# Kernel tuning notes

Hardware: AMD Instinct MI355X
Metric: run time of the kernel (lower is better)

The kernel has to match this reference:

```python
import jax, jax.numpy as jnp
import numpy as np

L, N, H, SQ = 24, 16384, 128, 32
D_OP, D_ATTR, D_FILT, D_OUT = 16, 56, 74, 32
D_IN = 2 * SQ + D_OP + D_ATTR  # 136
EPS = 1e-5
SLOPE = 0.01  # LeakyReLU default


def setup_inputs() -> dict:
    key = jax.random.key(0)
    ks = jax.random.split(key, 24)
    f32 = jnp.float32
    inp = {
        'op_pad': jax.random.normal(ks[0], (L, N, D_OP), f32),
        'attr_pad': jax.random.normal(ks[1], (L, N, D_ATTR), f32),
        'filter_pad': jax.random.normal(ks[2], (L, N, D_FILT), f32),
        'output_pad': jax.random.normal(ks[3], (L, N, D_OUT), f32),
        'mapping_pad': jax.random.randint(ks[4], (L, N, 2), 0, N + 1, jnp.int32),
        'batch_size': 4096,
        # filter / output squeeze linears
        'Wf': jax.random.normal(ks[5], (SQ, D_FILT), f32) * 0.05,
        'bf': jax.random.normal(ks[6], (SQ,), f32) * 0.05,
        'Wo': jax.random.normal(ks[7], (SQ, D_OUT), f32) * 0.05,
        'bo': jax.random.normal(ks[8], (SQ,), f32) * 0.05,
        # batchnorm affine params
        'g1': jnp.ones((SQ,), f32), 'beta1': jnp.zeros((SQ,), f32),
        'g2': jnp.ones((SQ,), f32), 'beta2': jnp.zeros((SQ,), f32),
        # LSTM (PyTorch layout: gates i,f,g,o stacked)
        'Wih': jax.random.normal(ks[9], (4 * H, D_IN), f32) * 0.05,
        'Whh': jax.random.normal(ks[10], (4 * H, H), f32) * 0.05,
        'bih': jax.random.normal(ks[11], (4 * H,), f32) * 0.05,
        'bhh': jax.random.normal(ks[12], (4 * H,), f32) * 0.05,
        # final MLP head
        'W1': jax.random.normal(ks[13], (20, H), f32) * 0.05,
        'b1': jax.random.normal(ks[14], (20,), f32) * 0.05,
        'W2': jax.random.normal(ks[15], (1, 20), f32) * 0.05,
        'b2': jax.random.normal(ks[16], (1,), f32) * 0.05,
    }
    return inp


def _leaky(x):
    return jnp.where(x > 0, x, SLOPE * x)


def _bn(x, g, b):
    # BatchNorm1d in training mode: batch stats (biased var), eps=1e-5
    m = jnp.mean(x, axis=0)
    v = jnp.var(x, axis=0)
    return (x - m) * jax.lax.rsqrt(v + EPS) * g + b


def _forward(op_pad, attr_pad, filter_pad, output_pad, mapping_pad, batch_size,
             Wf, bf, Wo, bo, g1, beta1, g2, beta2, Wih, Whh, bih, bhh, W1, b1, W2, b2):
    l, n = op_pad.shape[0], op_pad.shape[1]
    # squeeze filter / output features, flattened over (L*N)
    fd = _bn(_leaky(filter_pad.reshape(l * n, -1) @ Wf.T + bf), g1, beta1).reshape(l, n, SQ)
    od = _bn(_leaky(output_pad.reshape(l * n, -1) @ Wo.T + bo), g2, beta2).reshape(l, n, SQ)
    lstm_in = jnp.concatenate([op_pad, attr_pad, fd, od], axis=2)  # [L,N,D_IN]

    def step(carry, xs):
        h, c = carry                       # [N,H] previous level states
        x, mapping = xs                    # [N,D_IN], [N,2]
        mask = (mapping != 0)[..., None]   # [N,2,1]
        idx = jnp.maximum(mapping - 1, 0)  # [N,2] gather indices
        gh = jnp.sum(jnp.where(mask, h[idx], 0.0), axis=1) * 0.5  # [N,H]
        gc = jnp.sum(jnp.where(mask, c[idx], 0.0), axis=1) * 0.5
        gates = x @ Wih.T + bih + gh @ Whh.T + bhh  # [N,4H]
        i, f, g, o = jnp.split(gates, 4, axis=1)
        c_new = jax.nn.sigmoid(f) * gc + jax.nn.sigmoid(i) * jnp.tanh(g)
        h_new = jax.nn.sigmoid(o) * jnp.tanh(c_new)
        return (h_new, c_new), None

    z = jnp.zeros((n, H), lstm_in.dtype)
    # loop goes from the deepest level (index L-1) up to 0
    (h, _), _ = jax.lax.scan(step, (z, z), (lstm_in[::-1], mapping_pad[::-1]))
    out = h[:batch_size]
    out = jax.nn.sigmoid((out @ W1.T + b1) @ W2.T + b2)  # [B,1]
    return out


def reference(op_pad, attr_pad, filter_pad, output_pad, mapping_pad, batch_size,
              Wf, bf, Wo, bo, g1, beta1, g2, beta2, Wih, Whh, bih, bhh, W1, b1, W2, b2):
    return _forward(op_pad, attr_pad, filter_pad, output_pad, mapping_pad, batch_size,
                    Wf, bf, Wo, bo, g1, beta1, g2, beta2, Wih, Whh, bih, bhh, W1, b1, W2, b2)
```

## Files before the change

kernel.cpp:

```cpp
#include <hip/hip_runtime.h>
#include <hip/hip_bf16.h>

#define LL 24
#define NN 16384
#define HH 128
#define KP 288
#define LN (LL*NN)

typedef __bf16 bf16;
typedef __attribute__((ext_vector_type(8))) __bf16 bf16x8;
typedef __attribute__((ext_vector_type(2))) __bf16 bf16x2;
typedef __attribute__((ext_vector_type(4))) float f32x4;

__device__ __forceinline__ float sigm(float x){ return 1.f/(1.f+__expf(-x)); }
__device__ __forceinline__ float tanhfast(float x){
    float e = __expf(-2.f*fabsf(x));
    float t = (1.f-e)/(1.f+e);
    return x >= 0.f ? t : -t;
}
__device__ __forceinline__ void gld16(const void* g, void* l){
    __builtin_amdgcn_global_load_lds(
        (const __attribute__((address_space(1))) void*)g,
        (__attribute__((address_space(3))) void*)l, 16, 0, 0);
}

template<int D>
__global__ __launch_bounds__(256) void act_kernel(
    const float* __restrict__ X, const float* __restrict__ W,
    const float* __restrict__ bias, bf16* __restrict__ act,
    float* __restrict__ sums)
{
    __shared__ float w_lds[D*32];
    __shared__ float xs[128*D];
    const int tid = threadIdx.x;
    for (int i = tid; i < D*32; i += 256) {
        int k = i >> 5, ch = i & 31;
        w_lds[i] = W[ch*D + k];
    }
    const int c2 = tid & 15;
    const int rg = tid >> 4;
    const int ch0 = 2*c2, ch1 = ch0+1;
    const float b0 = bias[ch0], b1 = bias[ch1];
    float s0=0.f,s1=0.f,q0=0.f,q1=0.f;
    for (int tile = blockIdx.x; tile < LN/128; tile += gridDim.x) {
        const long row0 = (long)tile*128;
        __syncthreads();
        for (int i = tid; i < 128*D; i += 256) xs[i] = X[row0*D + i];
        __syncthreads();
        float a0[8], a1[8];
        #pragma unroll
        for (int i=0;i<8;++i){ a0[i]=b0; a1[i]=b1; }
        for (int k=0;k<D;++k){
            float w0 = w_lds[(k<<5)+ch0];
            float w1 = w_lds[(k<<5)+ch1];
            #pragma unroll
            for (int i=0;i<8;++i){
                float x = xs[(rg*8+i)*D + k];
                a0[i] = fmaf(x,w0,a0[i]);
                a1[i] = fmaf(x,w1,a1[i]);
            }
        }
        #pragma unroll
        for (int i=0;i<8;++i){
            float v0 = a0[i]; v0 = v0>0.f ? v0 : 0.01f*v0;
            float v1 = a1[i]; v1 = v1>0.f ? v1 : 0.01f*v1;
            bf16x2 pk; pk[0]=(bf16)v0; pk[1]=(bf16)v1;
            *(bf16x2*)&act[(row0 + rg*8+i)*32 + ch0] = pk;
            s0+=v0; q0+=v0*v0; s1+=v1; q1+=v1*v1;
        }
    }
    __syncthreads();
    float* red = xs;
    red[tid]=s0; red[256+tid]=q0; red[512+tid]=s1; red[768+tid]=q1;
    __syncthreads();
    if (tid < 16) {
        float ts0=0,tq0=0,ts1=0,tq1=0;
        for (int r=0;r<16;++r){
            int t = (r<<4) | tid;
            ts0+=red[t]; tq0+=red[256+t]; ts1+=red[512+t]; tq1+=red[768+t];
        }
        atomicAdd(&sums[2*tid],      ts0);
        atomicAdd(&sums[2*tid+1],    ts1);
        atomicAdd(&sums[32+2*tid],   tq0);
        atomicAdd(&sums[32+2*tid+1], tq1);
    }
}

__global__ void prep_wtb(const float* __restrict__ Wih, const float* __restrict__ Whh,
                         const float* __restrict__ bih, const float* __restrict__ bhh,
                         bf16* __restrict__ Wtb, float* __restrict__ b4p)
{
    const int np = blockIdx.x;
    const int k  = threadIdx.x;
    const int gate = (np>>4)&3;
    const int j = gate*128 + (np>>6)*16 + (np&15);
    if (k < KP) {
        float v = 0.f;
        if (k < 136)      v = Wih[(long)j*136 + k];
        else if (k >= 160) v = Whh[(long)j*128 + (k-160)];
        Wtb[(long)np*KP + k] = (bf16)v;
    }
    if (k == 0) b4p[np] = bih[j] + bhh[j];
}

__global__ void prep_stats(const float* __restrict__ stats,
    const float* __restrict__ g1, const float* __restrict__ beta1,
    const float* __restrict__ g2, const float* __restrict__ beta2,
    const float* __restrict__ W1, const float* __restrict__ b1,
    const float* __restrict__ W2, const float* __restrict__ b2,
    float* __restrict__ ss, float* __restrict__ wvb)
{
    const int t = threadIdx.x;
    const float inv = 1.f/(float)LN;
    if (t < 32) {
        float mean = stats[t]*inv;
        float var  = stats[32+t]*inv - mean*mean;
        float sc = g1[t]/sqrtf(var + 1e-5f);
        ss[t] = sc; ss[32+t] = beta1[t] - mean*sc;
    } else if (t < 64) {
        int c = t - 32;
        float mean = stats[64+c]*inv;
        float var  = stats[96+c]*inv - mean*mean;
        float sc = g2[c]/sqrtf(var + 1e-5f);
        ss[64+c] = sc; ss[96+c] = beta2[c] - mean*sc;
    }
    float s = 0.f;
    for (int a=0;a<20;++a) s += W2[a]*W1[a*HH + t];
    wvb[t] = s;
    if (t == 0) {
        float sb = 0.f;
        for (int a=0;a<20;++a) sb += W2[a]*b1[a];
        wvb[128] = sb + b2[0];
    }
}

__global__ __launch_bounds__(256) void build_a(
    const float* __restrict__ op, const float* __restrict__ attr,
    const bf16* __restrict__ actf, const bf16* __restrict__ acto,
    const int* __restrict__ map, const float* __restrict__ ss,
    const bf16* __restrict__ h_prev, bf16* __restrict__ A,
    int l, int first)
{
    const int n0 = blockIdx.x * 32;
    const long lbase = (long)l * NN;
    for (int i = threadIdx.x; i < 32*36; i += 256) {
        const int r = i / 36, c = i - r*36;
        const long n = n0 + r;
        const long e = lbase + n;
        const int k0 = c*8;
        bf16x8 out;
        if (c < 9) {
            const float* src = (c < 2) ? (op + e*16 + k0) : (attr + e*56 + (k0-16));
            float4 f0 = *(const float4*)src;
            float4 f1 = *(const float4*)(src+4);
            out[0]=(bf16)f0.x; out[1]=(bf16)f0.y; out[2]=(bf16)f0.z; out[3]=(bf16)f0.w;
            out[4]=(bf16)f1.x; out[5]=(bf16)f1.y; out[6]=(bf16)f1.z; out[7]=(bf16)f1.w;
        } else if (c < 17) {
            const int ch = (c < 13) ? (k0-72) : (k0-104);
            const bf16* src = (c < 13) ? (actf + e*32 + ch) : (acto + e*32 + ch);
            const float* s = ss + ((c < 13) ? 0 : 64);
            bf16x8 v = *(const bf16x8*)src;
            #pragma unroll
            for (int j=0;j<8;++j)
                out[j] = (bf16)fmaf((float)v[j], s[ch+j], s[32+ch+j]);
        } else if (c < 20) {
            #pragma unroll
            for (int j=0;j<8;++j) out[j] = (bf16)0.f;
        } else {
            const int jj = k0 - 160;
            float g[8] = {0,0,0,0,0,0,0,0};
            if (!first) {
                int2 mp = *(const int2*)&map[e*2];
                if (mp.x) { bf16x8 v = *(const bf16x8*)&h_prev[(long)(mp.x-1)*HH + jj];
                    #pragma unroll
                    for (int j=0;j<8;++j) g[j] += (float)v[j]; }
                if (mp.y) { bf16x8 v = *(const bf16x8*)&h_prev[(long)(mp.y-1)*HH + jj];
                    #pragma unroll
                    for (int j=0;j<8;++j) g[j] += (float)v[j]; }
            }
            #pragma unroll
            for (int j=0;j<8;++j) out[j] = (bf16)(0.5f*g[j]);
        }
        *(bf16x8*)&A[n*KP + k0] = out;
    }
}

__global__ __launch_bounds__(256) void lstm_gemm(
    const bf16* __restrict__ A, const bf16* __restrict__ Wtb,
    const float* __restrict__ b4p, const int* __restrict__ map,
    const float* __restrict__ c_prev, float* __restrict__ c_next,
    bf16* __restrict__ h_next, int l, int first)
{
    __shared__ bf16 As[128*32];
    __shared__ bf16 Bs[128*32];
    const int tid  = threadIdx.x;
    const int bm   = blockIdx.x;
    const int bn   = blockIdx.y;
    const int m0   = bm*128, n0p = bn*128;
    const int lane = tid & 63, w = tid >> 6;
    const int wr   = w >> 1,  wc = w & 1;

    f32x4 acc[4][4];
    #pragma unroll
    for (int ni=0; ni<4; ++ni){
        float b = b4p[n0p + wc*64 + ni*16 + (lane&15)];
        #pragma unroll
        for (int mi=0; mi<4; ++mi) acc[mi][ni] = (f32x4){b,b,b,b};
    }

    const bf16* Ab = A   + (size_t)m0*KP;
    const bf16* Bb = Wtb + (size_t)n0p*KP;
    const int lrr = lane >> 2;
    const int qs  = lane & 3;

    for (int kk=0; kk<9; ++kk){
        __syncthreads();
        #pragma unroll
        for (int hh=0; hh<2; ++hh){
            const int lr = w*32 + hh*16 + lrr;
            const int q  = qs ^ ((lr>>1)&3);
            const size_t go = (size_t)lr*KP + kk*32 + q*8;
            gld16(Ab + go, &As[(w*32 + hh*16)*32]);
            gld16(Bb + go, &Bs[(w*32 + hh*16)*32]);
        }
        __syncthreads();
        bf16x8 af[4], bfr[4];
        #pragma unroll
        for (int t4=0; t4<4; ++t4){
            const int am = wr*64 + t4*16 + (lane&15);
            af[t4] = *(const bf16x8*)&As[am*32 + (((lane>>4) ^ ((am>>1)&3))<<3)];
            const int bn_ = wc*64 + t4*16 + (lane&15);
            bfr[t4] = *(const bf16x8*)&Bs[bn_*32 + (((lane>>4) ^ ((bn_>>1)&3))<<3)];
        }
        #pragma unroll
        for (int mi=0; mi<4; ++mi)
            #pragma unroll
            for (int ni=0; ni<4; ++ni)
                acc[mi][ni] = __builtin_amdgcn_mfma_f32_16x16x32_bf16(
                    af[mi], bfr[ni], acc[mi][ni], 0, 0, 0);
    }

    const long lbase = (long)l * NN;
    const int cell = bn*32 + wc*16 + (lane&15);
    #pragma unroll
    for (int mi=0; mi<4; ++mi){
        const int rbase = m0 + wr*64 + mi*16 + (lane>>4)*4;
        #pragma unroll
        for (int reg=0; reg<4; ++reg){
            const int n = rbase + reg;
            float gc = 0.f;
            if (!first){
                int2 mp = *(const int2*)&map[(lbase+n)*2];
                if (mp.x) gc += c_prev[(long)(mp.x-1)*HH + cell];
                if (mp.y) gc += c_prev[(long)(mp.y-1)*HH + cell];
                gc *= 0.5f;
            }
            float cn = sigm(acc[mi][1][reg])*gc
                     + sigm(acc[mi][0][reg])*tanhfast(acc[mi][2][reg]);
            float hn = sigm(acc[mi][3][reg])*tanhfast(cn);
            c_next[(long)n*HH + cell] = cn;
            h_next[(long)n*HH + cell] = (bf16)hn;
        }
    }
}

__global__ __launch_bounds__(256) void final_k(
    const bf16* __restrict__ h, const float* __restrict__ wvb,
    float* __restrict__ out, int rows)
{
    int gt = blockIdx.x*256 + threadIdx.x;
    int row = gt >> 6;
    int lane = gt & 63;
    if (row >= rows) return;
    float v = fmaf((float)h[(long)row*HH + lane], wvb[lane],
                   (float)h[(long)row*HH + 64 + lane] * wvb[64+lane]);
    #pragma unroll
    for (int off=32; off>0; off>>=1) v += __shfl_down(v, off);
    if (lane == 0) out[row] = sigm(v + wvb[128]);
}

extern "C" void kernel_launch(void* const* d_in, const int* in_sizes, int n_in,
                              void* d_out, int out_size, void* d_ws, size_t ws_size,
                              hipStream_t stream)
{
    const float* op      = (const float*)d_in[0];
    const float* attr    = (const float*)d_in[1];
    const float* filt    = (const float*)d_in[2];
    const float* outp    = (const float*)d_in[3];
    const int*   mapping = (const int*)d_in[4];
    const float* Wf  = (const float*)d_in[6];
    const float* bf_ = (const float*)d_in[7];
    const float* Wo  = (const float*)d_in[8];
    const float* bo  = (const float*)d_in[9];
    const float* g1  = (const float*)d_in[10];
    const float* be1 = (const float*)d_in[11];
    const float* g2  = (const float*)d_in[12];
    const float* be2 = (const float*)d_in[13];
    const float* Wih = (const float*)d_in[14];
    const float* Whh = (const float*)d_in[15];
    const float* bih = (const float*)d_in[16];
    const float* bhh = (const float*)d_in[17];
    const float* W1  = (const float*)d_in[18];
    const float* b1  = (const float*)d_in[19];
    const float* W2  = (const float*)d_in[20];
    const float* b2  = (const float*)d_in[21];

    char* p = (char*)d_ws;
    auto alloc = [&](size_t bytes){ char* r = p; p += (bytes + 255) & ~255ull; return r; };
    bf16* actf = (bf16*)alloc((size_t)LN*32*2);
    bf16* acto = (bf16*)alloc((size_t)LN*32*2);
    bf16* h0   = (bf16*)alloc((size_t)NN*HH*2);
    bf16* h1   = (bf16*)alloc((size_t)NN*HH*2);
    float* c0  = (float*)alloc((size_t)NN*HH*4);
    float* c1  = (float*)alloc((size_t)NN*HH*4);
    bf16* Abuf = (bf16*)alloc((size_t)NN*KP*2);
    bf16* Wtb  = (bf16*)alloc((size_t)512*KP*2);
    float* b4p = (float*)alloc(512*4);
    float* stats=(float*)alloc(128*4);
    float* ssb = (float*)alloc(128*4);
    float* wvb = (float*)alloc(132*4);

    hipMemsetAsync(stats, 0, 128*sizeof(float), stream);
    act_kernel<74><<<768, 256, 0, stream>>>(filt, Wf, bf_, actf, stats);
    act_kernel<32><<<768, 256, 0, stream>>>(outp, Wo, bo, acto, stats+64);
    prep_wtb<<<512, 320, 0, stream>>>(Wih, Whh, bih, bhh, Wtb, b4p);
    prep_stats<<<1, 128, 0, stream>>>(stats, g1, be1, g2, be2, W1, b1, W2, b2, ssb, wvb);

    bf16*  hb[2] = {h0, h1};
    float* cb[2] = {c0, c1};
    for (int t = 0; t < LL; ++t) {
        const int l = (LL-1) - t;
        const int first = (t == 0);
        build_a<<<NN/32, 256, 0, stream>>>(op, attr, actf, acto, mapping, ssb,
                                           hb[t&1], Abuf, l, first);
        lstm_gemm<<<dim3(128,4), 256, 0, stream>>>(Abuf, Wtb, b4p, mapping,
            cb[t&1], cb[(t+1)&1], hb[(t+1)&1], l, first);
    }
    final_k<<<(out_size*64 + 255)/256, 256, 0, stream>>>(hb[0], wvb, (float*)d_out, out_size);
}
```

Measured before the change: 1.340 ms.

## Retile squeeze-linear kernels with float4 register blocking and padded LDS rows

Rewrites the filter/output squeeze-linear activation kernel so each thread computes a 6x4 output block. Weights are read as float4 directly from global memory (cached), and inputs come from a padded LDS tile of 192 rows read as float4. The goal is fewer LDS loads per FMA and fewer bank conflicts than the old scalar 8x2 scheme. The BN statistics reduction and grid sizes are reworked to match. This adds register pressure and zero-padding logic for K=74, which is not a multiple of 4.

```diff
diff --git a/kernel.cpp b/kernel.cpp
--- a/kernel.cpp
+++ b/kernel.cpp
@@ -9,6 +9,7 @@
 
 typedef __bf16 bf16;
 typedef __attribute__((ext_vector_type(8))) __bf16 bf16x8;
+typedef __attribute__((ext_vector_type(4))) __bf16 bf16x4;
 typedef __attribute__((ext_vector_type(2))) __bf16 bf16x2;
 typedef __attribute__((ext_vector_type(4))) float f32x4;
 
@@ -24,65 +25,104 @@
         (__attribute__((address_space(3))) void*)l, 16, 0, 0);
 }
 
-template<int D>
+template<int D, int DP, int NQ, int TILES>
 __global__ __launch_bounds__(256) void act_kernel(
     const float* __restrict__ X, const float* __restrict__ W,
     const float* __restrict__ bias, bf16* __restrict__ act,
     float* __restrict__ sums)
 {
-    __shared__ float w_lds[D*32];
-    __shared__ float xs[128*D];
+    __shared__ float xs[192*DP];
     const int tid = threadIdx.x;
-    for (int i = tid; i < D*32; i += 256) {
-        int k = i >> 5, ch = i & 31;
-        w_lds[i] = W[ch*D + k];
-    }
-    const int c2 = tid & 15;
-    const int rg = tid >> 4;
-    const int ch0 = 2*c2, ch1 = ch0+1;
-    const float b0 = bias[ch0], b1 = bias[ch1];
-    float s0=0.f,s1=0.f,q0=0.f,q1=0.f;
-    for (int tile = blockIdx.x; tile < LN/128; tile += gridDim.x) {
-        const long row0 = (long)tile*128;
+    const int cg  = tid & 7;
+    const int rg  = tid >> 3;
+    const int rbase = rg*6;
+
+    float bc[4];
+    #pragma unroll
+    for (int c=0;c<4;++c) bc[c] = bias[cg*4+c];
+
+    float s[4] = {0,0,0,0}, qq[4] = {0,0,0,0};
+
+    for (int tile = blockIdx.x; tile < TILES; tile += gridDim.x) {
         __syncthreads();
-        for (int i = tid; i < 128*D; i += 256) xs[i] = X[row0*D + i];
+        const float* Xt = X + (size_t)tile * (192*D);
+        for (int i = tid; i < 192*D; i += 256) {
+            int r = i / D, c = i - r*D;
+            xs[r*DP + c] = Xt[i];
+        }
+        if constexpr (4*NQ > D) {
+            constexpr int PADW = 4*NQ - D;
+            for (int i = tid; i < 192*PADW; i += 256) {
+                int r = i / PADW, c = i - r*PADW;
+                xs[r*DP + D + c] = 0.f;
+            }
+        }
         __syncthreads();
-        float a0[8], a1[8];
-        #pragma unroll
-        for (int i=0;i<8;++i){ a0[i]=b0; a1[i]=b1; }
-        for (int k=0;k<D;++k){
-            float w0 = w_lds[(k<<5)+ch0];
-            float w1 = w_lds[(k<<5)+ch1];
-            #pragma unroll
-            for (int i=0;i<8;++i){
-                float x = xs[(rg*8+i)*D + k];
-                a0[i] = fmaf(x,w0,a0[i]);
-                a1[i] = fmaf(x,w1,a1[i]);
-            }
-        }
-        #pragma unroll
-        for (int i=0;i<8;++i){
-            float v0 = a0[i]; v0 = v0>0.f ? v0 : 0.01f*v0;
-            float v1 = a1[i]; v1 = v1>0.f ? v1 : 0.01f*v1;
-            bf16x2 pk; pk[0]=(bf16)v0; pk[1]=(bf16)v1;
-            *(bf16x2*)&act[(row0 + rg*8+i)*32 + ch0] = pk;
-            s0+=v0; q0+=v0*v0; s1+=v1; q1+=v1*v1;
-        }
-    }
+
+        float a[6][4];
+        #pragma unroll
+        for (int i=0;i<6;++i)
+            #pragma unroll
+            for (int c=0;c<4;++c) a[i][c] = 0.f;
+
+        #pragma unroll 2
+        for (int q = 0; q < NQ; ++q) {
+            float4 wv[4];
+            #pragma unroll
+            for (int c = 0; c < 4; ++c) {
+                const float* wp = W + (cg*4 + c)*D + q*4;
+                if constexpr (D % 4 == 0) {
+                    wv[c] = *(const float4*)wp;
+                } else {
+                    if ((4*NQ > D) && (q == NQ-1)) {
+                        float2 lo = *(const float2*)wp;
+                        wv[c] = make_float4(lo.x, lo.y, 0.f, 0.f);
+                    } else {
+                        float2 lo = *(const float2*)wp;
+                        float2 hi = *(const float2*)(wp+2);
+                        wv[c] = make_float4(lo.x, lo.y, hi.x, hi.y);
+                    }
+                }
+            }
+            #pragma unroll
+            for (int i = 0; i < 6; ++i) {
+                float4 xv = *(const float4*)&xs[(rbase+i)*DP + q*4];
+                #pragma unroll
+                for (int c = 0; c < 4; ++c) {
+                    a[i][c] = fmaf(xv.x, wv[c].x, a[i][c]);
+                    a[i][c] = fmaf(xv.y, wv[c].y, a[i][c]);
+                    a[i][c] = fmaf(xv.z, wv[c].z, a[i][c]);
+                    a[i][c] = fmaf(xv.w, wv[c].w, a[i][c]);
+                }
+            }
+        }
+
+        #pragma unroll
+        for (int i = 0; i < 6; ++i) {
+            bf16x4 pk;
+            #pragma unroll
+            for (int c = 0; c < 4; ++c) {
+                float v = a[i][c] + bc[c];
+                v = v > 0.f ? v : 0.01f*v;
+                pk[c] = (bf16)v;
+                s[c] += v; qq[c] += v*v;
+            }
+            *(bf16x4*)&act[((size_t)tile*192 + rbase + i)*32 + cg*4] = pk;
+        }
+    }
+
     __syncthreads();
     float* red = xs;
-    red[tid]=s0; red[256+tid]=q0; red[512+tid]=s1; red[768+tid]=q1;
+    #pragma unroll
+    for (int c=0;c<4;++c){ red[tid*8 + c*2] = s[c]; red[tid*8 + c*2 + 1] = qq[c]; }
     __syncthreads();
-    if (tid < 16) {
-        float ts0=0,tq0=0,ts1=0,tq1=0;
-        for (int r=0;r<16;++r){
-            int t = (r<<4) | tid;
-            ts0+=red[t]; tq0+=red[256+t]; ts1+=red[512+t]; tq1+=red[768+t];
-        }
-        atomicAdd(&sums[2*tid],      ts0);
-        atomicAdd(&sums[2*tid+1],    ts1);
-        atomicAdd(&sums[32+2*tid],   tq0);
-        atomicAdd(&sums[32+2*tid+1], tq1);
+    if (tid < 64) {
+        const int ch = tid >> 1, v = tid & 1;
+        const int cgr = ch >> 2, cl = ch & 3;
+        float t = 0.f;
+        for (int r = 0; r < 32; ++r)
+            t += red[(r*8 + cgr)*8 + cl*2 + v];
+        atomicAdd(&sums[v*32 + ch], t);
     }
 }
 
@@ -321,8 +361,8 @@
     float* wvb = (float*)alloc(132*4);
 
     hipMemsetAsync(stats, 0, 128*sizeof(float), stream);
-    act_kernel<74><<<768, 256, 0, stream>>>(filt, Wf, bf_, actf, stats);
-    act_kernel<32><<<768, 256, 0, stream>>>(outp, Wo, bo, acto, stats+64);
+    act_kernel<74, 84, 19, 2048><<<512, 256, 0, stream>>>(filt, Wf, bf_, actf, stats);
+    act_kernel<32, 36,  8, 2048><<<1024, 256, 0, stream>>>(outp, Wo, bo, acto, stats+64);
     prep_wtb<<<512, 320, 0, stream>>>(Wih, Whh, bih, bhh, Wtb, b4p);
     prep_stats<<<1, 128, 0, stream>>>(stats, g1, be1, g2, be2, W1, b1, W2, b2, ssb, wvb);
 
```

After: 1.370 ms. +2.2%, slower.
